# Kernel tuning notes

Measured on AMD Instinct MI355X. Metric: run time of the kernel, lower is better.

The kernel has to match this reference:

```python
import jax, jax.numpy as jnp
import numpy as np

D_MODEL = 1024
EXPAND = 2
D_INNER = EXPAND * D_MODEL   # 2048
D_STATE = 16
D_CONV = 4
DT_RANK = 64                  # ceil(d_model / 16)
BATCH = 2
SEQLEN = 1024
DT_MIN, DT_MAX = 0.001, 0.1


def setup_inputs() -> dict:
    key = jax.random.key(0)
    ks = jax.random.split(key, 10)
    s = 0.02
    # dt bias init per Mamba: inv-softplus of dt sampled log-uniform in [dt_min, dt_max]
    u = jax.random.uniform(ks[0], (D_INNER,), jnp.float32)
    dt = jnp.exp(u * (np.log(DT_MAX) - np.log(DT_MIN)) + np.log(DT_MIN))
    dt = jnp.clip(dt, 1e-4, None)
    inv_dt = dt + jnp.log(-jnp.expm1(-dt))
    dt_std = DT_RANK ** -0.5
    A_log = jnp.log(jnp.tile(jnp.arange(1, D_STATE + 1, dtype=jnp.float32), (D_INNER, 1)))
    return {
        "hidden_states": jax.random.normal(ks[1], (BATCH, SEQLEN, D_MODEL), jnp.float32),
        "in_proj_w": jax.random.normal(ks[2], (2 * D_INNER, D_MODEL), jnp.float32) * s,
        "conv1d_w": jax.random.normal(ks[3], (D_INNER, D_CONV), jnp.float32) * s,
        "conv1d_b": jnp.zeros((D_INNER,), jnp.float32),
        "x_proj_w": jax.random.normal(ks[4], (DT_RANK + 2 * D_STATE, D_INNER), jnp.float32) * s,
        "dt_proj_w": jax.random.uniform(ks[5], (D_INNER, DT_RANK), jnp.float32, -dt_std, dt_std),
        "dt_proj_b": inv_dt,
        "A_log": A_log,
        "D_skip": jnp.ones((D_INNER,), jnp.float32),
        "out_proj_w": jax.random.normal(ks[6], (D_MODEL, D_INNER), jnp.float32) * s,
    }


def _mamba_forward(hidden_states, in_proj_w, conv1d_w, conv1d_b, x_proj_w,
                   dt_proj_w, dt_proj_b, A_log, D_skip, out_proj_w):
    B_, L, _ = hidden_states.shape
    # in_proj: (b, l, d_model) -> (b, l, 2*d_inner); split into x and gate z
    xz = jnp.einsum('bld,ed->ble', hidden_states, in_proj_w)
    x, z = xz[..., :D_INNER], xz[..., D_INNER:]
    # causal depthwise conv1d over time (pad left K-1, truncate to L) + SiLU
    xp = jnp.pad(x, ((0, 0), (D_CONV - 1, 0), (0, 0)))
    xc = conv1d_b
    acc = jnp.zeros_like(x)
    for k in range(D_CONV):  # tiny fixed kernel loop
        acc = acc + conv1d_w[:, k] * xp[:, k:k + L, :]
    xc = jax.nn.silu(acc + conv1d_b)
    # input-dependent dt / B / C
    x_dbl = jnp.einsum('bld,rd->blr', xc, x_proj_w)
    dt_lr = x_dbl[..., :DT_RANK]
    Bm = x_dbl[..., DT_RANK:DT_RANK + D_STATE]        # (b, l, n)
    Cm = x_dbl[..., DT_RANK + D_STATE:]               # (b, l, n)
    delta = jax.nn.softplus(jnp.einsum('blr,dr->bld', dt_lr, dt_proj_w) + dt_proj_b)
    A = -jnp.exp(A_log)                               # (d, n)

    def step(state, inputs):
        delta_t, B_t, C_t, u_t = inputs               # (b,d) (b,n) (b,n) (b,d)
        dA = jnp.exp(delta_t[..., None] * A)          # (b, d, n)
        state = state * dA + (delta_t * u_t)[..., None] * B_t[:, None, :]
        y_t = jnp.einsum('bdn,bn->bd', state, C_t)
        return state, y_t

    init = jnp.zeros((B_, D_INNER, D_STATE), delta.dtype)
    scan_in = (jnp.swapaxes(delta, 0, 1), jnp.swapaxes(Bm, 0, 1),
               jnp.swapaxes(Cm, 0, 1), jnp.swapaxes(xc, 0, 1))
    _, ys = jax.lax.scan(step, init, scan_in)         # ys: (l, b, d)
    y = jnp.swapaxes(ys, 0, 1)
    y = y + xc * D_skip                               # skip connection
    y = y * jax.nn.silu(z)                            # gate
    return jnp.einsum('bld,md->blm', y, out_proj_w)   # out_proj (no bias)


def reference(hidden_states, in_proj_w, conv1d_w, conv1d_b, x_proj_w,
              dt_proj_w, dt_proj_b, A_log, D_skip, out_proj_w):
    return _mamba_forward(hidden_states, in_proj_w, conv1d_w, conv1d_b, x_proj_w,
                          dt_proj_w, dt_proj_b, A_log, D_skip, out_proj_w)
```

## Files before the change

### kernel.cpp

```cpp
#include <hip/hip_runtime.h>
#include <hip/hip_bf16.h>
#include <math.h>
#include <stdint.h>

#define D_MODEL 1024
#define D_INNER 2048
#define D_STATE 16
#define D_CONV  4
#define DT_RANK 64
#define BATCH   2
#define SEQLEN  1024
#define M_TOK   (BATCH * SEQLEN)
#define XDBL_W  (DT_RANK + 2 * D_STATE)
#define CHUNKS  64
#define CLEN    (SEQLEN / CHUNKS)
#define KSPLIT  8

typedef unsigned short us16;
typedef __bf16 bf16x8 __attribute__((ext_vector_type(8)));
typedef float floatx4 __attribute__((ext_vector_type(4)));

__device__ __forceinline__ float silu_f(float v) {
    return v / (1.0f + __expf(-v));
}
__device__ __forceinline__ float softplus_f(float v) {
    return v > 20.0f ? v : log1pf(__expf(v));
}
__device__ __forceinline__ us16 f2bf(float f) {
    unsigned u = __float_as_uint(f);
    u += 0x7FFF + ((u >> 16) & 1);
    return (us16)(u >> 16);
}
__device__ __forceinline__ float bf2f(us16 h) {
    return __uint_as_float(((unsigned)h) << 16);
}

__device__ __forceinline__ void gload_lds16(const us16* g, us16* l) {
    auto* l3 = reinterpret_cast<__attribute__((address_space(3))) us16*>(
        reinterpret_cast<uintptr_t>(l));
    auto* g1 = reinterpret_cast<const __attribute__((address_space(1))) us16*>(
        reinterpret_cast<uintptr_t>(g));
    __builtin_amdgcn_global_load_lds(g1, l3, 16, 0, 0);
}

__global__ __launch_bounds__(256)
void split_bf16(const float* __restrict__ src, us16* __restrict__ hi,
                us16* __restrict__ lo) {
    const int i = (blockIdx.x * 256 + threadIdx.x) * 4;
    const float4 v = *(const float4*)(src + i);
    us16 h0 = f2bf(v.x), h1 = f2bf(v.y), h2 = f2bf(v.z), h3 = f2bf(v.w);
    ushort4 hv = {h0, h1, h2, h3};
    ushort4 lv = {f2bf(v.x - bf2f(h0)), f2bf(v.y - bf2f(h1)),
                  f2bf(v.z - bf2f(h2)), f2bf(v.w - bf2f(h3))};
    *(ushort4*)(hi + i) = hv;
    *(ushort4*)(lo + i) = lv;
}

template<int BN, int MODE>
__global__ __launch_bounds__(256)
void gemm_mfma3(const us16* __restrict__ Ah, const us16* __restrict__ Al,
                const us16* __restrict__ Wh, const us16* __restrict__ Wl,
                int lda, int kLen, float* __restrict__ C0,
                float* __restrict__ C1, int ldc)
{
    constexpr int BM = 128;
    constexpr int NT = BN / 32;
    __shared__ us16 sAh[BM * 32];
    __shared__ us16 sAl[BM * 32];
    __shared__ us16 sWh[BN * 32];
    __shared__ us16 sWl[BN * 32];

    const int tid  = threadIdx.x;
    const int wave = tid >> 6;
    const int lane = tid & 63;
    const int wm   = wave & 1;
    const int wn   = wave >> 1;
    const int m0   = blockIdx.y * BM;
    const int n0   = blockIdx.x * BN;
    const int kBeg = blockIdx.z * kLen;
    const int quad = lane >> 4;
    const int l15  = lane & 15;
    const int sr   = lane >> 2;
    const int spos = lane & 3;

    floatx4 acc[4][NT] = {};

    for (int k0 = 0; k0 < kLen; k0 += 32) {
        __syncthreads();
        {
            int s = wave;
            int row = s * 16 + sr;
            int c = spos ^ ((row >> 1) & 3);
            size_t go = (size_t)(m0 + row) * lda + kBeg + k0 + c * 8;
            gload_lds16(Ah + go, sAh + s * 512);
            gload_lds16(Al + go, sAl + s * 512);
            s = wave + 4;
            row = s * 16 + sr;
            c = spos ^ ((row >> 1) & 3);
            go = (size_t)(m0 + row) * lda + kBeg + k0 + c * 8;
            gload_lds16(Ah + go, sAh + s * 512);
            gload_lds16(Al + go, sAl + s * 512);
        }
        {
            int s = wave;
            int row = s * 16 + sr;
            int c = spos ^ ((row >> 1) & 3);
            size_t go = (size_t)(n0 + row) * lda + kBeg + k0 + c * 8;
            gload_lds16(Wh + go, sWh + s * 512);
            gload_lds16(Wl + go, sWl + s * 512);
            if (BN == 128) {
                s = wave + 4;
                row = s * 16 + sr;
                c = spos ^ ((row >> 1) & 3);
                go = (size_t)(n0 + row) * lda + kBeg + k0 + c * 8;
                gload_lds16(Wh + go, sWh + s * 512);
                gload_lds16(Wl + go, sWl + s * 512);
            }
        }
        __syncthreads();

        bf16x8 ah[4], al[4], bh[NT], bl[NT];
#pragma unroll
        for (int i = 0; i < 4; i++) {
            const int r = wm * 64 + i * 16 + l15;
            const int off = r * 32 + ((quad ^ ((r >> 1) & 3)) * 8);
            ah[i] = *(const bf16x8*)(sAh + off);
            al[i] = *(const bf16x8*)(sAl + off);
        }
#pragma unroll
        for (int j = 0; j < NT; j++) {
            const int r = wn * (BN / 2) + j * 16 + l15;
            const int off = r * 32 + ((quad ^ ((r >> 1) & 3)) * 8);
            bh[j] = *(const bf16x8*)(sWh + off);
            bl[j] = *(const bf16x8*)(sWl + off);
        }
#pragma unroll
        for (int i = 0; i < 4; i++)
#pragma unroll
            for (int j = 0; j < NT; j++) {
                acc[i][j] = __builtin_amdgcn_mfma_f32_16x16x32_bf16(
                    ah[i], bh[j], acc[i][j], 0, 0, 0);
                acc[i][j] = __builtin_amdgcn_mfma_f32_16x16x32_bf16(
                    al[i], bh[j], acc[i][j], 0, 0, 0);
                acc[i][j] = __builtin_amdgcn_mfma_f32_16x16x32_bf16(
                    ah[i], bl[j], acc[i][j], 0, 0, 0);
            }
    }

#pragma unroll
    for (int i = 0; i < 4; i++) {
        const int rowb = m0 + wm * 64 + i * 16 + quad * 4;
#pragma unroll
        for (int j = 0; j < NT; j++) {
            const int col = n0 + wn * (BN / 2) + j * 16 + l15;
#pragma unroll
            for (int r = 0; r < 4; r++) {
                const float v = acc[i][j][r];
                const size_t rr = (size_t)(rowb + r);
                if (MODE == 1) {
                    if (n0 < D_INNER) C0[rr * D_INNER + col] = v;
                    else              C1[rr * D_INNER + (col - D_INNER)] = v;
                } else {
                    C0[((size_t)blockIdx.z * M_TOK + rr) * ldc + col] = v;
                }
            }
        }
    }
}

__global__ __launch_bounds__(256)
void add2_kernel(const float* __restrict__ part, float* __restrict__ out)
{
    const int i = (blockIdx.x * 256 + threadIdx.x) * 4;
    float4 a = *(const float4*)(part + i);
    const float4 b = *(const float4*)(part + (size_t)M_TOK * D_MODEL + i);
    a.x += b.x; a.y += b.y; a.z += b.z; a.w += b.w;
    *(float4*)(out + i) = a;
}

template<int MODE>
__global__ __launch_bounds__(256)
void gemm_nt(const float* __restrict__ A, int lda,
             const float* __restrict__ W, int ldw,
             float* __restrict__ C0, float* __restrict__ C1, int ldc,
             const float* __restrict__ bias,
             int M, int N, int K)
{
    __shared__ float As[16][68];
    __shared__ float Ws[16][68];

    const int tid  = threadIdx.x;
    const int tx   = tid & 15;
    const int ty   = tid >> 4;
    const int n0   = blockIdx.x * 64;
    const int m0   = blockIdx.y * 64;
    const int lrow = tid >> 2;
    const int lkq  = tid & 3;

    float acc[4][4] = {};

    for (int k0 = 0; k0 < K; k0 += 16) {
        const float4 av = *(const float4*)(A + (size_t)(m0 + lrow) * lda + k0 + lkq * 4);
        const int wn = n0 + lrow;
        float4 wv = make_float4(0.f, 0.f, 0.f, 0.f);
        if (wn < N)
            wv = *(const float4*)(W + (size_t)wn * ldw + k0 + lkq * 4);

        __syncthreads();
        As[lkq * 4 + 0][lrow] = av.x;
        As[lkq * 4 + 1][lrow] = av.y;
        As[lkq * 4 + 2][lrow] = av.z;
        As[lkq * 4 + 3][lrow] = av.w;
        Ws[lkq * 4 + 0][lrow] = wv.x;
        Ws[lkq * 4 + 1][lrow] = wv.y;
        Ws[lkq * 4 + 2][lrow] = wv.z;
        Ws[lkq * 4 + 3][lrow] = wv.w;
        __syncthreads();

#pragma unroll
        for (int k = 0; k < 16; k++) {
            const float4 a = *(const float4*)&As[k][ty * 4];
            const float4 w = *(const float4*)&Ws[k][tx * 4];
            const float avv[4] = {a.x, a.y, a.z, a.w};
            const float wvv[4] = {w.x, w.y, w.z, w.w};
#pragma unroll
            for (int i = 0; i < 4; i++)
#pragma unroll
                for (int j = 0; j < 4; j++)
                    acc[i][j] += avv[i] * wvv[j];
        }
    }

    const int mbase = m0 + ty * 4;
    const int nbase = n0 + tx * 4;
#pragma unroll
    for (int i = 0; i < 4; i++) {
#pragma unroll
        for (int j = 0; j < 4; j++) {
            const int n = nbase + j;
            const size_t row = (size_t)(mbase + i);
            if (MODE == 0) {
                if (n < N) C0[row * ldc + n] = acc[i][j];
            } else if (MODE == 2) {
                C0[row * ldc + n] = softplus_f(acc[i][j] + bias[n]);
            }
        }
    }
}

__global__ __launch_bounds__(256)
void gemm_xproj(const float* __restrict__ A, const float* __restrict__ W,
                float* __restrict__ part)
{
    __shared__ float As[16][68];
    __shared__ float Ws[16][68];

    const int tid  = threadIdx.x;
    const int tx   = tid & 15;
    const int ty   = tid >> 4;
    const int n0   = blockIdx.x * 64;
    const int m0   = blockIdx.y * 64;
    const int kz   = blockIdx.z;
    const int lrow = tid >> 2;
    const int lkq  = tid & 3;

    float acc[4][4] = {};
    const int kbeg = kz * (D_INNER / KSPLIT);
    const int kend = kbeg + (D_INNER / KSPLIT);

    for (int k0 = kbeg; k0 < kend; k0 += 16) {
        const float4 av = *(const float4*)(A + (size_t)(m0 + lrow) * D_INNER + k0 + lkq * 4);
        const int wn = n0 + lrow;
        float4 wv = make_float4(0.f, 0.f, 0.f, 0.f);
        if (wn < XDBL_W)
            wv = *(const float4*)(W + (size_t)wn * D_INNER + k0 + lkq * 4);

        __syncthreads();
        As[lkq * 4 + 0][lrow] = av.x;
        As[lkq * 4 + 1][lrow] = av.y;
        As[lkq * 4 + 2][lrow] = av.z;
        As[lkq * 4 + 3][lrow] = av.w;
        Ws[lkq * 4 + 0][lrow] = wv.x;
        Ws[lkq * 4 + 1][lrow] = wv.y;
        Ws[lkq * 4 + 2][lrow] = wv.z;
        Ws[lkq * 4 + 3][lrow] = wv.w;
        __syncthreads();

#pragma unroll
        for (int k = 0; k < 16; k++) {
            const float4 a = *(const float4*)&As[k][ty * 4];
            const float4 w = *(const float4*)&Ws[k][tx * 4];
            const float avv[4] = {a.x, a.y, a.z, a.w};
            const float wvv[4] = {w.x, w.y, w.z, w.w};
#pragma unroll
            for (int i = 0; i < 4; i++)
#pragma unroll
                for (int j = 0; j < 4; j++)
                    acc[i][j] += avv[i] * wvv[j];
        }
    }

    const int mbase = m0 + ty * 4;
    const int nbase = n0 + tx * 4;
#pragma unroll
    for (int i = 0; i < 4; i++)
#pragma unroll
        for (int j = 0; j < 4; j++) {
            const int n = nbase + j;
            if (n < XDBL_W)
                part[((size_t)kz * M_TOK + mbase + i) * XDBL_W + n] = acc[i][j];
        }
}

__global__ __launch_bounds__(256)
void xproj_reduce(const float* __restrict__ part, float* __restrict__ xdbl)
{
    const int i = blockIdx.x * 256 + threadIdx.x;
    float s = 0.f;
#pragma unroll
    for (int k = 0; k < KSPLIT; k++)
        s += part[(size_t)k * M_TOK * XDBL_W + i];
    xdbl[i] = s;
}

__global__ __launch_bounds__(256)
void conv_silu_kernel(const float* __restrict__ x, const float* __restrict__ w,
                      const float* __restrict__ bias, float* __restrict__ xc)
{
    const int idx = blockIdx.x * 256 + threadIdx.x;
    const int d = idx & (D_INNER - 1);
    const int t = (idx >> 11) & (SEQLEN - 1);
    const int b = idx >> 21;
    float acc = bias[d];
#pragma unroll
    for (int k = 0; k < D_CONV; k++) {
        const int tt = t - (D_CONV - 1) + k;
        if (tt >= 0)
            acc += w[d * D_CONV + k] * x[((size_t)b * SEQLEN + tt) * D_INNER + d];
    }
    xc[idx] = silu_f(acc);
}

__global__ __launch_bounds__(256)
void scan_part(const float* __restrict__ delta, const float* __restrict__ xdbl,
               const float* __restrict__ xc, const float* __restrict__ A_log,
               float* __restrict__ P, float* __restrict__ S)
{
    const int g = blockIdx.x * 256 + threadIdx.x;
    const int d = g & (D_INNER - 1);
    const int c = (g >> 11) & (CHUNKS - 1);
    const int b = g >> 17;

    float An[D_STATE];
#pragma unroll
    for (int n = 0; n < D_STATE; n++)
        An[n] = -__expf(A_log[d * D_STATE + n]);

    float p[D_STATE], s[D_STATE];
#pragma unroll
    for (int n = 0; n < D_STATE; n++) { p[n] = 1.f; s[n] = 0.f; }

    const size_t row0 = (size_t)b * SEQLEN + c * CLEN;
#pragma unroll 4
    for (int t = 0; t < CLEN; t++) {
        const size_t row = row0 + t;
        const float dlt  = delta[row * D_INNER + d];
        const float dltu = dlt * xc[row * D_INNER + d];
        const float4* Bp = (const float4*)(xdbl + row * XDBL_W + DT_RANK);
        const float4 B0 = Bp[0], B1 = Bp[1], B2 = Bp[2], B3 = Bp[3];
        const float Bv[D_STATE] = {B0.x, B0.y, B0.z, B0.w, B1.x, B1.y, B1.z, B1.w,
                                   B2.x, B2.y, B2.z, B2.w, B3.x, B3.y, B3.z, B3.w};
#pragma unroll
        for (int n = 0; n < D_STATE; n++) {
            const float a = __expf(dlt * An[n]);
            s[n] = s[n] * a + dltu * Bv[n];
            p[n] *= a;
        }
    }

    const size_t base = ((size_t)(b * CHUNKS + c) * D_STATE) * D_INNER + d;
#pragma unroll
    for (int n = 0; n < D_STATE; n++) {
        P[base + (size_t)n * D_INNER] = p[n];
        S[base + (size_t)n * D_INNER] = s[n];
    }
}

__global__ __launch_bounds__(256)
void scan_prefix(float* PH, const float* __restrict__ S)
{
    const int g = blockIdx.x * 256 + threadIdx.x;
    const int d = g & (D_INNER - 1);
    const int n = (g >> 11) & (D_STATE - 1);
    const int b = g >> 15;

    float h = 0.f;
    for (int c = 0; c < CHUNKS; c++) {
        const size_t idx = ((size_t)(b * CHUNKS + c) * D_STATE + n) * D_INNER + d;
        const float p = PH[idx];
        const float s = S[idx];
        PH[idx] = h;
        h = s + p * h;
    }
}

__global__ __launch_bounds__(256)
void scan_apply(const float* __restrict__ delta, const float* __restrict__ xdbl,
                const float* __restrict__ xc, const float* __restrict__ A_log,
                const float* __restrict__ D_skip,
                const float* __restrict__ H,
                const float* __restrict__ z,
                us16* __restrict__ yh, us16* __restrict__ yl)
{
    const int g = blockIdx.x * 256 + threadIdx.x;
    const int d = g & (D_INNER - 1);
    const int c = (g >> 11) & (CHUNKS - 1);
    const int b = g >> 17;

    float An[D_STATE];
#pragma unroll
    for (int n = 0; n < D_STATE; n++)
        An[n] = -__expf(A_log[d * D_STATE + n]);

    float st[D_STATE];
    const size_t hbase = ((size_t)(b * CHUNKS + c) * D_STATE) * D_INNER + d;
#pragma unroll
    for (int n = 0; n < D_STATE; n++)
        st[n] = H[hbase + (size_t)n * D_INNER];

    const float Dv = D_skip[d];
    const size_t row0 = (size_t)b * SEQLEN + c * CLEN;
#pragma unroll 4
    for (int t = 0; t < CLEN; t++) {
        const size_t row = row0 + t;
        const float dlt  = delta[row * D_INNER + d];
        const float u    = xc[row * D_INNER + d];
        const float dltu = dlt * u;
        const float4* Bp = (const float4*)(xdbl + row * XDBL_W + DT_RANK);
        const float4 B0 = Bp[0], B1 = Bp[1], B2 = Bp[2], B3 = Bp[3];
        const float4* Cp = (const float4*)(xdbl + row * XDBL_W + DT_RANK + D_STATE);
        const float4 C0 = Cp[0], C1 = Cp[1], C2 = Cp[2], C3 = Cp[3];
        const float Bv[D_STATE] = {B0.x, B0.y, B0.z, B0.w, B1.x, B1.y, B1.z, B1.w,
                                   B2.x, B2.y, B2.z, B2.w, B3.x, B3.y, B3.z, B3.w};
        const float Cv[D_STATE] = {C0.x, C0.y, C0.z, C0.w, C1.x, C1.y, C1.z, C1.w,
                                   C2.x, C2.y, C2.z, C2.w, C3.x, C3.y, C3.z, C3.w};
        float y = 0.f;
#pragma unroll
        for (int n = 0; n < D_STATE; n++) {
            const float a = __expf(dlt * An[n]);
            st[n] = st[n] * a + dltu * Bv[n];
            y += st[n] * Cv[n];
        }
        const float yv = (y + u * Dv) * silu_f(z[row * D_INNER + d]);
        const us16 h = f2bf(yv);
        yh[row * D_INNER + d] = h;
        yl[row * D_INNER + d] = f2bf(yv - bf2f(h));
    }
}

extern "C" void kernel_launch(void* const* d_in, const int* in_sizes, int n_in,
                              void* d_out, int out_size, void* d_ws, size_t ws_size,
                              hipStream_t stream)
{
    const float* hs         = (const float*)d_in[0];
    const float* in_proj_w  = (const float*)d_in[1];
    const float* conv_w     = (const float*)d_in[2];
    const float* conv_b     = (const float*)d_in[3];
    const float* x_proj_w   = (const float*)d_in[4];
    const float* dt_proj_w  = (const float*)d_in[5];
    const float* dt_proj_b  = (const float*)d_in[6];
    const float* A_log      = (const float*)d_in[7];
    const float* D_skip     = (const float*)d_in[8];
    const float* out_proj_w = (const float*)d_in[9];
    float* out = (float*)d_out;

    char* base = (char*)d_ws;
    const size_t MB = 1u << 20;
    float* xbuf  = (float*)(base);
    float* zbuf  = (float*)(base + 16 * MB);
    float* xcbuf = (float*)(base + 32 * MB);
    float* opart = (float*)(base + 32 * MB);
    float* xdbl  = (float*)(base + 48 * MB);
    us16*  iwh   = (us16*)(base + 49 * MB);
    us16*  iwl   = (us16*)(base + 57 * MB);
    float* Pbuf  = (float*)(base + 49 * MB);
    float* Sbuf  = (float*)(base + 65 * MB);
    us16*  ybh   = (us16*)(base + 65 * MB);
    us16*  ybl   = (us16*)(base + 73 * MB);
    us16*  hsh   = (us16*)(base + 81 * MB);
    us16*  hsl   = (us16*)(base + 85 * MB);
    float* part  = (float*)(base + 81 * MB);
    us16*  owh   = (us16*)(base + 81 * MB);
    us16*  owl   = (us16*)(base + 85 * MB);

    const dim3 blk(256);

    split_bf16<<<(M_TOK * D_MODEL) / 1024, blk, 0, stream>>>(hs, hsh, hsl);
    split_bf16<<<(2 * D_INNER * D_MODEL) / 1024, blk, 0, stream>>>(in_proj_w, iwh, iwl);

    gemm_mfma3<128, 1><<<dim3((2 * D_INNER) / 128, M_TOK / 128), blk, 0, stream>>>(
        hsh, hsl, iwh, iwl, D_MODEL, D_MODEL, xbuf, zbuf, D_INNER);

    conv_silu_kernel<<<(BATCH * SEQLEN * D_INNER) / 256, blk, 0, stream>>>(
        xbuf, conv_w, conv_b, xcbuf);

    gemm_xproj<<<dim3(2, M_TOK / 64, KSPLIT), blk, 0, stream>>>(
        xcbuf, x_proj_w, part);
    xproj_reduce<<<(M_TOK * XDBL_W) / 256, blk, 0, stream>>>(part, xdbl);

    split_bf16<<<(D_MODEL * D_INNER) / 1024, blk, 0, stream>>>(out_proj_w, owh, owl);

    gemm_nt<2><<<dim3(D_INNER / 64, M_TOK / 64), blk, 0, stream>>>(
        xdbl, XDBL_W, dt_proj_w, DT_RANK, xbuf, nullptr, D_INNER, dt_proj_b,
        M_TOK, D_INNER, DT_RANK);

    scan_part<<<(BATCH * CHUNKS * D_INNER) / 256, blk, 0, stream>>>(
        xbuf, xdbl, xcbuf, A_log, Pbuf, Sbuf);
    scan_prefix<<<(BATCH * D_STATE * D_INNER) / 256, blk, 0, stream>>>(
        Pbuf, Sbuf);
    scan_apply<<<(BATCH * CHUNKS * D_INNER) / 256, blk, 0, stream>>>(
        xbuf, xdbl, xcbuf, A_log, D_skip, Pbuf, zbuf, ybh, ybl);

    gemm_mfma3<64, 2><<<dim3(D_MODEL / 64, M_TOK / 128, 2), blk, 0, stream>>>(
        ybh, ybl, owh, owl, D_INNER, D_INNER / 2, opart, nullptr, D_MODEL);
    add2_kernel<<<(M_TOK * D_MODEL) / 1024, blk, 0, stream>>>(opart, out);
}
```

Measured before the change: 336.9 us.

## Fuse causal conv+SiLU into x_proj GEMM and scan kernels; merge bf16 splits

Removes the standalone conv_silu kernel and its 16 MB intermediate buffer. The causal depthwise conv plus SiLU is now recomputed on the fly wherever its output is consumed: in the x_proj GEMM A-tile load and in both scan passes, which keep a rolling window of three previous inputs. The three bf16 hi/lo split launches are merged into one kernel, and the workspace is relaid out so delta gets its own buffer instead of overwriting xbuf. The cost is extra conv arithmetic and extra loads of the preceding rows in the GEMM loader, in exchange for one fewer full write and read of the intermediate plus fewer launches.

New measurement: 330.0 us. -2.0%, faster.

```diff
diff --git a/kernel.cpp b/kernel.cpp
--- a/kernel.cpp
+++ b/kernel.cpp
@@ -44,9 +44,20 @@
 }
 
 __global__ __launch_bounds__(256)
-void split_bf16(const float* __restrict__ src, us16* __restrict__ hi,
-                us16* __restrict__ lo) {
-    const int i = (blockIdx.x * 256 + threadIdx.x) * 4;
+void split_all(const float* __restrict__ hs, const float* __restrict__ iw,
+               const float* __restrict__ ow,
+               us16* __restrict__ hsh, us16* __restrict__ hsl,
+               us16* __restrict__ iwh, us16* __restrict__ iwl,
+               us16* __restrict__ owh, us16* __restrict__ owl)
+{
+    const int b = blockIdx.x;
+    const float* src;
+    us16 *hi, *lo;
+    int rel;
+    if (b < 2048)      { src = hs; hi = hsh; lo = hsl; rel = b; }
+    else if (b < 6144) { src = iw; hi = iwh; lo = iwl; rel = b - 2048; }
+    else               { src = ow; hi = owh; lo = owl; rel = b - 6144; }
+    const int i = (rel * 256 + threadIdx.x) * 4;
     const float4 v = *(const float4*)(src + i);
     us16 h0 = f2bf(v.x), h1 = f2bf(v.y), h2 = f2bf(v.z), h3 = f2bf(v.w);
     ushort4 hv = {h0, h1, h2, h3};
@@ -178,13 +189,11 @@
     *(float4*)(out + i) = a;
 }
 
-template<int MODE>
-__global__ __launch_bounds__(256)
-void gemm_nt(const float* __restrict__ A, int lda,
+__global__ __launch_bounds__(256)
+void gemm_dt(const float* __restrict__ A, int lda,
              const float* __restrict__ W, int ldw,
-             float* __restrict__ C0, float* __restrict__ C1, int ldc,
-             const float* __restrict__ bias,
-             int M, int N, int K)
+             float* __restrict__ C0, int ldc,
+             const float* __restrict__ bias, int K)
 {
     __shared__ float As[16][68];
     __shared__ float Ws[16][68];
@@ -201,10 +210,7 @@
 
     for (int k0 = 0; k0 < K; k0 += 16) {
         const float4 av = *(const float4*)(A + (size_t)(m0 + lrow) * lda + k0 + lkq * 4);
-        const int wn = n0 + lrow;
-        float4 wv = make_float4(0.f, 0.f, 0.f, 0.f);
-        if (wn < N)
-            wv = *(const float4*)(W + (size_t)wn * ldw + k0 + lkq * 4);
+        const float4 wv = *(const float4*)(W + (size_t)(n0 + lrow) * ldw + k0 + lkq * 4);
 
         __syncthreads();
         As[lkq * 4 + 0][lrow] = av.x;
@@ -234,23 +240,18 @@
     const int mbase = m0 + ty * 4;
     const int nbase = n0 + tx * 4;
 #pragma unroll
-    for (int i = 0; i < 4; i++) {
+    for (int i = 0; i < 4; i++)
 #pragma unroll
         for (int j = 0; j < 4; j++) {
             const int n = nbase + j;
-            const size_t row = (size_t)(mbase + i);
-            if (MODE == 0) {
-                if (n < N) C0[row * ldc + n] = acc[i][j];
-            } else if (MODE == 2) {
-                C0[row * ldc + n] = softplus_f(acc[i][j] + bias[n]);
-            }
-        }
-    }
-}
-
-__global__ __launch_bounds__(256)
-void gemm_xproj(const float* __restrict__ A, const float* __restrict__ W,
-                float* __restrict__ part)
+            C0[(size_t)(mbase + i) * ldc + n] = softplus_f(acc[i][j] + bias[n]);
+        }
+}
+
+__global__ __launch_bounds__(256)
+void gemm_xproj(const float* __restrict__ xg, const float* __restrict__ conv_w,
+                const float* __restrict__ conv_b,
+                const float* __restrict__ W, float* __restrict__ part)
 {
     __shared__ float As[16][68];
     __shared__ float Ws[16][68];
@@ -264,12 +265,34 @@
     const int lrow = tid >> 2;
     const int lkq  = tid & 3;
 
+    const float4* cw = (const float4*)conv_w;
+    const float4* cb = (const float4*)conv_b;
+
     float acc[4][4] = {};
     const int kbeg = kz * (D_INNER / KSPLIT);
     const int kend = kbeg + (D_INNER / KSPLIT);
 
+    const int m = m0 + lrow;
+    const int t = m & (SEQLEN - 1);
+
     for (int k0 = kbeg; k0 < kend; k0 += 16) {
-        const float4 av = *(const float4*)(A + (size_t)(m0 + lrow) * D_INNER + k0 + lkq * 4);
+        const int dcol = k0 + lkq * 4;
+        const float4 w0 = cw[dcol], w1 = cw[dcol + 1], w2 = cw[dcol + 2], w3 = cw[dcol + 3];
+        float4 a = cb[dcol >> 2];
+        const float* xr = xg + (size_t)m * D_INNER + dcol;
+        {
+            float4 xk;
+            if (t >= 3) { xk = *(const float4*)(xr - 3 * D_INNER);
+                a.x += w0.x * xk.x; a.y += w1.x * xk.y; a.z += w2.x * xk.z; a.w += w3.x * xk.w; }
+            if (t >= 2) { xk = *(const float4*)(xr - 2 * D_INNER);
+                a.x += w0.y * xk.x; a.y += w1.y * xk.y; a.z += w2.y * xk.z; a.w += w3.y * xk.w; }
+            if (t >= 1) { xk = *(const float4*)(xr - 1 * D_INNER);
+                a.x += w0.z * xk.x; a.y += w1.z * xk.y; a.z += w2.z * xk.z; a.w += w3.z * xk.w; }
+            xk = *(const float4*)(xr);
+            a.x += w0.w * xk.x; a.y += w1.w * xk.y; a.z += w2.w * xk.z; a.w += w3.w * xk.w;
+        }
+        const float4 av = make_float4(silu_f(a.x), silu_f(a.y), silu_f(a.z), silu_f(a.w));
+
         const int wn = n0 + lrow;
         float4 wv = make_float4(0.f, 0.f, 0.f, 0.f);
         if (wn < XDBL_W)
@@ -288,10 +311,10 @@
 
 #pragma unroll
         for (int k = 0; k < 16; k++) {
-            const float4 a = *(const float4*)&As[k][ty * 4];
-            const float4 w = *(const float4*)&Ws[k][tx * 4];
-            const float avv[4] = {a.x, a.y, a.z, a.w};
-            const float wvv[4] = {w.x, w.y, w.z, w.w};
+            const float4 a4 = *(const float4*)&As[k][ty * 4];
+            const float4 w4 = *(const float4*)&Ws[k][tx * 4];
+            const float avv[4] = {a4.x, a4.y, a4.z, a4.w};
+            const float wvv[4] = {w4.x, w4.y, w4.z, w4.w};
 #pragma unroll
             for (int i = 0; i < 4; i++)
 #pragma unroll
@@ -324,26 +347,9 @@
 }
 
 __global__ __launch_bounds__(256)
-void conv_silu_kernel(const float* __restrict__ x, const float* __restrict__ w,
-                      const float* __restrict__ bias, float* __restrict__ xc)
-{
-    const int idx = blockIdx.x * 256 + threadIdx.x;
-    const int d = idx & (D_INNER - 1);
-    const int t = (idx >> 11) & (SEQLEN - 1);
-    const int b = idx >> 21;
-    float acc = bias[d];
-#pragma unroll
-    for (int k = 0; k < D_CONV; k++) {
-        const int tt = t - (D_CONV - 1) + k;
-        if (tt >= 0)
-            acc += w[d * D_CONV + k] * x[((size_t)b * SEQLEN + tt) * D_INNER + d];
-    }
-    xc[idx] = silu_f(acc);
-}
-
-__global__ __launch_bounds__(256)
 void scan_part(const float* __restrict__ delta, const float* __restrict__ xdbl,
-               const float* __restrict__ xc, const float* __restrict__ A_log,
+               const float* __restrict__ xg, const float* __restrict__ conv_w,
+               const float* __restrict__ conv_b, const float* __restrict__ A_log,
                float* __restrict__ P, float* __restrict__ S)
 {
     const int g = blockIdx.x * 256 + threadIdx.x;
@@ -356,16 +362,30 @@
     for (int n = 0; n < D_STATE; n++)
         An[n] = -__expf(A_log[d * D_STATE + n]);
 
+    const float4 wd = ((const float4*)conv_w)[d];
+    const float cb = conv_b[d];
+
     float p[D_STATE], s[D_STATE];
 #pragma unroll
     for (int n = 0; n < D_STATE; n++) { p[n] = 1.f; s[n] = 0.f; }
 
     const size_t row0 = (size_t)b * SEQLEN + c * CLEN;
+    const float* xp = xg + row0 * D_INNER + d;
+    float xm3 = 0.f, xm2 = 0.f, xm1 = 0.f;
+    if (c > 0) {
+        xm3 = xp[-3 * D_INNER];
+        xm2 = xp[-2 * D_INNER];
+        xm1 = xp[-1 * D_INNER];
+    }
+
 #pragma unroll 4
     for (int t = 0; t < CLEN; t++) {
         const size_t row = row0 + t;
+        const float xm0 = xp[(size_t)t * D_INNER];
+        const float u   = silu_f(cb + wd.x * xm3 + wd.y * xm2 + wd.z * xm1 + wd.w * xm0);
+        xm3 = xm2; xm2 = xm1; xm1 = xm0;
         const float dlt  = delta[row * D_INNER + d];
-        const float dltu = dlt * xc[row * D_INNER + d];
+        const float dltu = dlt * u;
         const float4* Bp = (const float4*)(xdbl + row * XDBL_W + DT_RANK);
         const float4 B0 = Bp[0], B1 = Bp[1], B2 = Bp[2], B3 = Bp[3];
         const float Bv[D_STATE] = {B0.x, B0.y, B0.z, B0.w, B1.x, B1.y, B1.z, B1.w,
@@ -406,7 +426,8 @@
 
 __global__ __launch_bounds__(256)
 void scan_apply(const float* __restrict__ delta, const float* __restrict__ xdbl,
-                const float* __restrict__ xc, const float* __restrict__ A_log,
+                const float* __restrict__ xg, const float* __restrict__ conv_w,
+                const float* __restrict__ conv_b, const float* __restrict__ A_log,
                 const float* __restrict__ D_skip,
                 const float* __restrict__ H,
                 const float* __restrict__ z,
@@ -422,6 +443,9 @@
     for (int n = 0; n < D_STATE; n++)
         An[n] = -__expf(A_log[d * D_STATE + n]);
 
+    const float4 wd = ((const float4*)conv_w)[d];
+    const float cb = conv_b[d];
+
     float st[D_STATE];
     const size_t hbase = ((size_t)(b * CHUNKS + c) * D_STATE) * D_INNER + d;
 #pragma unroll
@@ -430,11 +454,21 @@
 
     const float Dv = D_skip[d];
     const size_t row0 = (size_t)b * SEQLEN + c * CLEN;
+    const float* xp = xg + row0 * D_INNER + d;
+    float xm3 = 0.f, xm2 = 0.f, xm1 = 0.f;
+    if (c > 0) {
+        xm3 = xp[-3 * D_INNER];
+        xm2 = xp[-2 * D_INNER];
+        xm1 = xp[-1 * D_INNER];
+    }
+
 #pragma unroll 4
     for (int t = 0; t < CLEN; t++) {
         const size_t row = row0 + t;
+        const float xm0 = xp[(size_t)t * D_INNER];
+        const float u   = silu_f(cb + wd.x * xm3 + wd.y * xm2 + wd.z * xm1 + wd.w * xm0);
+        xm3 = xm2; xm2 = xm1; xm1 = xm0;
         const float dlt  = delta[row * D_INNER + d];
-        const float u    = xc[row * D_INNER + d];
         const float dltu = dlt * u;
         const float4* Bp = (const float4*)(xdbl + row * XDBL_W + DT_RANK);
         const float4 B0 = Bp[0], B1 = Bp[1], B2 = Bp[2], B3 = Bp[3];
@@ -478,48 +512,42 @@
     const size_t MB = 1u << 20;
     float* xbuf  = (float*)(base);
     float* zbuf  = (float*)(base + 16 * MB);
-    float* xcbuf = (float*)(base + 32 * MB);
+    float* dbuf  = (float*)(base + 32 * MB);
     float* opart = (float*)(base + 32 * MB);
     float* xdbl  = (float*)(base + 48 * MB);
     us16*  iwh   = (us16*)(base + 49 * MB);
     us16*  iwl   = (us16*)(base + 57 * MB);
+    float* part  = (float*)(base + 49 * MB);
     float* Pbuf  = (float*)(base + 49 * MB);
+    us16*  hsh   = (us16*)(base + 65 * MB);
+    us16*  hsl   = (us16*)(base + 69 * MB);
     float* Sbuf  = (float*)(base + 65 * MB);
     us16*  ybh   = (us16*)(base + 65 * MB);
     us16*  ybl   = (us16*)(base + 73 * MB);
-    us16*  hsh   = (us16*)(base + 81 * MB);
-    us16*  hsl   = (us16*)(base + 85 * MB);
-    float* part  = (float*)(base + 81 * MB);
     us16*  owh   = (us16*)(base + 81 * MB);
     us16*  owl   = (us16*)(base + 85 * MB);
 
     const dim3 blk(256);
 
-    split_bf16<<<(M_TOK * D_MODEL) / 1024, blk, 0, stream>>>(hs, hsh, hsl);
-    split_bf16<<<(2 * D_INNER * D_MODEL) / 1024, blk, 0, stream>>>(in_proj_w, iwh, iwl);
+    split_all<<<8192, blk, 0, stream>>>(hs, in_proj_w, out_proj_w,
+                                        hsh, hsl, iwh, iwl, owh, owl);
 
     gemm_mfma3<128, 1><<<dim3((2 * D_INNER) / 128, M_TOK / 128), blk, 0, stream>>>(
         hsh, hsl, iwh, iwl, D_MODEL, D_MODEL, xbuf, zbuf, D_INNER);
 
-    conv_silu_kernel<<<(BATCH * SEQLEN * D_INNER) / 256, blk, 0, stream>>>(
-        xbuf, conv_w, conv_b, xcbuf);
-
     gemm_xproj<<<dim3(2, M_TOK / 64, KSPLIT), blk, 0, stream>>>(
-        xcbuf, x_proj_w, part);
+        xbuf, conv_w, conv_b, x_proj_w, part);
     xproj_reduce<<<(M_TOK * XDBL_W) / 256, blk, 0, stream>>>(part, xdbl);
 
-    split_bf16<<<(D_MODEL * D_INNER) / 1024, blk, 0, stream>>>(out_proj_w, owh, owl);
-
-    gemm_nt<2><<<dim3(D_INNER / 64, M_TOK / 64), blk, 0, stream>>>(
-        xdbl, XDBL_W, dt_proj_w, DT_RANK, xbuf, nullptr, D_INNER, dt_proj_b,
-        M_TOK, D_INNER, DT_RANK);
+    gemm_dt<<<dim3(D_INNER / 64, M_TOK / 64), blk, 0, stream>>>(
+        xdbl, XDBL_W, dt_proj_w, DT_RANK, dbuf, D_INNER, dt_proj_b, DT_RANK);
 
     scan_part<<<(BATCH * CHUNKS * D_INNER) / 256, blk, 0, stream>>>(
-        xbuf, xdbl, xcbuf, A_log, Pbuf, Sbuf);
+        dbuf, xdbl, xbuf, conv_w, conv_b, A_log, Pbuf, Sbuf);
     scan_prefix<<<(BATCH * D_STATE * D_INNER) / 256, blk, 0, stream>>>(
         Pbuf, Sbuf);
     scan_apply<<<(BATCH * CHUNKS * D_INNER) / 256, blk, 0, stream>>>(
-        xbuf, xdbl, xcbuf, A_log, D_skip, Pbuf, zbuf, ybh, ybl);
+        dbuf, xdbl, xbuf, conv_w, conv_b, A_log, D_skip, Pbuf, zbuf, ybh, ybl);
 
     gemm_mfma3<64, 2><<<dim3(D_MODEL / 64, M_TOK / 128, 2), blk, 0, stream>>>(
         ybh, ybl, owh, owl, D_INNER, D_INNER / 2, opart, nullptr, D_MODEL);
```
